# Kernel optimization log

Measured on AMD Instinct MI355X. Metric: run time of the kernel, lower is better.

Reference implementation:

```python
import jax, jax.numpy as jnp
import numpy as np
import math

BS, SEQ, HID = 1, 2048, 2048
NH, NKV, HD = 32, 8, 64
BASE = 10000.0


def rotate_half(x):
    x1, x2 = x[..., : x.shape[-1] // 2], x[..., x.shape[-1] // 2 :]
    return jnp.concatenate((-x2, x1), axis=-1)


def setup_inputs() -> dict:
    key = jax.random.key(0)
    ks = jax.random.split(key, 6)
    s = 0.02
    return {
        "x": jax.random.normal(ks[0], (BS, SEQ, HID), dtype=jnp.float32),
        "attention_mask": jnp.zeros((BS, SEQ), dtype=jnp.float32),
        "position_ids": jnp.broadcast_to(jnp.arange(SEQ, dtype=jnp.int64 if jax.config.jax_enable_x64 else jnp.int32), (BS, SEQ)),
        "wq": jax.random.normal(ks[1], (HID, NH * HD), dtype=jnp.float32) * s,
        "wk": jax.random.normal(ks[2], (HID, NKV * HD), dtype=jnp.float32) * s,
        "wv": jax.random.normal(ks[3], (HID, NKV * HD), dtype=jnp.float32) * s,
        "wo": jax.random.normal(ks[4], (NH * HD, HID), dtype=jnp.float32) * s,
    }


def reference(x, attention_mask, position_ids, wq, wk, wv, wo):
    bs, seq, _ = x.shape
    groups = NH // NKV

    q = (x @ wq).reshape(bs, seq, NH, HD).transpose(0, 2, 1, 3)   # [b,H,S,D]
    k = (x @ wk).reshape(bs, seq, NKV, HD).transpose(0, 2, 1, 3)  # [b,Hkv,S,D]
    v = (x @ wv).reshape(bs, seq, NKV, HD).transpose(0, 2, 1, 3)

    # rotary embedding
    inv_freq = 1.0 / (BASE ** (jnp.arange(0, HD, 2, dtype=jnp.float32) / HD))  # [D/2]
    freqs = position_ids.astype(jnp.float32)[:, :, None] * inv_freq[None, None, :]  # [b,S,D/2]
    emb = jnp.concatenate((freqs, freqs), axis=-1)               # [b,S,D]
    cos = jnp.cos(emb)[:, None, :, :].astype(x.dtype)            # [b,1,S,D]
    sin = jnp.sin(emb)[:, None, :, :].astype(x.dtype)
    q = q * cos + rotate_half(q) * sin
    k = k * cos + rotate_half(k) * sin

    # repeat_kv (GQA expand)
    k = jnp.repeat(k, groups, axis=1)  # [b,H,S,D]
    v = jnp.repeat(v, groups, axis=1)

    scores = jnp.einsum("bhqd,bhkd->bhqk", q, k) / math.sqrt(HD)
    scores = scores + attention_mask[:, None, None, :]
    attn = jax.nn.softmax(scores.astype(jnp.float32), axis=-1).astype(q.dtype)
    out = jnp.einsum("bhqk,bhkd->bhqd", attn, v)                 # [b,H,S,D]
    out = out.transpose(0, 2, 1, 3).reshape(bs, seq, NH * HD)
    return out @ wo
```

## Files before the change

kernel.cpp:

```cpp
#include <hip/hip_runtime.h>

#define SEQ 2048
#define HID 2048
#define NH  32
#define NKV 8
#define HD  64

typedef _Float16 f16;
typedef __attribute__((ext_vector_type(4))) _Float16 f16x4;
typedef __attribute__((ext_vector_type(8))) _Float16 f16x8;
typedef __attribute__((ext_vector_type(2))) __fp16   h16x2;
typedef __attribute__((ext_vector_type(4))) float    f32x4;

__device__ __forceinline__ f32x4 mfma_16x16x32(f16x8 a, f16x8 b, f32x4 c) {
    return __builtin_amdgcn_mfma_f32_16x16x32_f16(a, b, c, 0, 0, 0);
}

__device__ __forceinline__ void async16(const void* g, void* l) {
    __builtin_amdgcn_global_load_lds(
        (const __attribute__((address_space(1))) void*)g,
        (__attribute__((address_space(3))) void*)l,
        16, 0, 0);
}

__global__ void prep_all(const float* __restrict__ x,
                         const float* __restrict__ wq, const float* __restrict__ wk,
                         const float* __restrict__ wv, const float* __restrict__ wo,
                         f16* __restrict__ xb,
                         f16* __restrict__ Wcat, f16* __restrict__ woT) {
    __shared__ float tile[32][33];
    int z = blockIdx.z;
    int tx = threadIdx.x, ty = threadIdx.y;
    if (z == 4) {
        int idx = (blockIdx.y * 64 + blockIdx.x) * 256 + ty * 32 + tx;
        int i = idx * 4;
        float4 v = *(const float4*)(x + i);
        f16x4 o = { (f16)v.x, (f16)v.y, (f16)v.z, (f16)v.w };
        *(f16x4*)(xb + i) = o;
        return;
    }
    const float* src; f16* dst; int C;
    if      (z == 0) { src = wq; dst = Wcat;                         C = 2048; }
    else if (z == 1) { src = wk; dst = Wcat + (size_t)2048 * 2048;   C = 512;  }
    else if (z == 2) { src = wv; dst = Wcat + (size_t)2560 * 2048;   C = 512;  }
    else             { src = wo; dst = woT;                          C = 2048; }
    int c0 = blockIdx.x * 32, r0 = blockIdx.y * 32;
    if (c0 >= C) return;
#pragma unroll
    for (int i = 0; i < 32; i += 8)
        tile[ty + i][tx] = src[(size_t)(r0 + ty + i) * C + c0 + tx];
    __syncthreads();
#pragma unroll
    for (int i = 0; i < 32; i += 8)
        dst[(size_t)(c0 + ty + i) * 2048 + r0 + tx] = (f16)tile[tx][ty + i];
}

template <int MODE>
__global__ __launch_bounds__(256)
void gemm_bt(const f16* __restrict__ A, const f16* __restrict__ BT,
             float* __restrict__ Cf, f16* __restrict__ Q, f16* __restrict__ Kk,
             f16* __restrict__ VT, const int* __restrict__ pos,
             const float* __restrict__ mask, int N, int K) {
    __shared__ f16 As[2][64 * 64];
    __shared__ f16 Bs[2][128 * 64];
    int t = threadIdx.x;
    int w = t >> 6, lane = t & 63, quad = lane >> 4, l15 = lane & 15;
    int wm = w >> 1, wn = w & 1;
    int m0 = blockIdx.y * 64, n0 = blockIdx.x * 128;
    int sw = l15 & 7;

    int r8 = lane >> 3;
    int cc = (lane & 7) ^ r8;
    const f16* Ag0 = A  + (size_t)(m0 + w * 16 + r8) * K + cc * 8;
    const f16* Ag1 = Ag0 + (size_t)8 * K;
    const f16* Bg  = BT + (size_t)(n0 + w * 32 + r8) * K + cc * 8;

    f32x4 acc[2][4] = {};

    async16(Ag0, &As[0][w * 1024]);
    async16(Ag1, &As[0][w * 1024 + 512]);
#pragma unroll
    for (int g = 0; g < 4; g++)
        async16(Bg + (size_t)(8 * g) * K, &Bs[0][w * 2048 + g * 512]);
    __syncthreads();

    int b = 0;
    for (int kt = 64; kt <= K; kt += 64) {
        if (kt < K) {
            async16(Ag0 + kt, &As[b ^ 1][w * 1024]);
            async16(Ag1 + kt, &As[b ^ 1][w * 1024 + 512]);
#pragma unroll
            for (int g = 0; g < 4; g++)
                async16(Bg + (size_t)(8 * g) * K + kt, &Bs[b ^ 1][w * 2048 + g * 512]);
        }
        f16x8 af[2][2], bf[4][2];
#pragma unroll
        for (int mi = 0; mi < 2; mi++) {
            int row = wm * 32 + mi * 16 + l15;
#pragma unroll
            for (int kh = 0; kh < 2; kh++)
                af[mi][kh] = *(const f16x8*)(&As[b][row * 64 + ((kh * 4 + quad) ^ sw) * 8]);
        }
#pragma unroll
        for (int ni = 0; ni < 4; ni++) {
            int row = wn * 64 + ni * 16 + l15;
#pragma unroll
            for (int kh = 0; kh < 2; kh++)
                bf[ni][kh] = *(const f16x8*)(&Bs[b][row * 64 + ((kh * 4 + quad) ^ sw) * 8]);
        }
#pragma unroll
        for (int mi = 0; mi < 2; mi++)
#pragma unroll
            for (int ni = 0; ni < 4; ni++) {
                acc[mi][ni] = mfma_16x16x32(af[mi][0], bf[ni][0], acc[mi][ni]);
                acc[mi][ni] = mfma_16x16x32(af[mi][1], bf[ni][1], acc[mi][ni]);
            }
        __syncthreads();
        b ^= 1;
    }

    int rb  = m0 + wm * 32 + quad * 4;
    int cbh = n0 + wn * 64;
    if (MODE == 0) {
        if (cbh < (NH + NKV) * HD) {
            bool isQ = cbh < NH * HD;
            f16* dst = isQ ? (Q  + (size_t)(cbh >> 6) * SEQ * HD)
                           : (Kk + (size_t)((cbh - NH * HD) >> 6) * SEQ * HD);
            float scale = isQ ? 0.18033688011112042f : 1.0f;
            float fr[2];
#pragma unroll
            for (int ni = 0; ni < 2; ni++)
                fr[ni] = __builtin_amdgcn_exp2f(
                    (float)(ni * 16 + l15) * -0.41524101186092029f);
#pragma unroll
            for (int mi = 0; mi < 2; mi++)
#pragma unroll
                for (int r = 0; r < 4; r++) {
                    int row = rb + mi * 16 + r;
                    float pv = (float)pos[row];
#pragma unroll
                    for (int ni = 0; ni < 2; ni++) {
                        float sn, cs;
                        __sincosf(pv * fr[ni], &sn, &cs);
                        float x1 = acc[mi][ni][r], x2 = acc[mi][ni + 2][r];
                        int d = ni * 16 + l15;
                        dst[(size_t)row * HD + d]      = (f16)(scale * (x1 * cs - x2 * sn));
                        dst[(size_t)row * HD + d + 32] = (f16)(scale * (x2 * cs + x1 * sn));
                    }
                }
        } else {
            const float LOG2E = 1.4426950408889634f;
#pragma unroll
            for (int mi = 0; mi < 2; mi++) {
                float4 mv = *(const float4*)(mask + rb + mi * 16);
                float em[4];
#pragma unroll
                for (int r = 0; r < 4; r++)
                    em[r] = __builtin_amdgcn_exp2f((&mv.x)[r] * LOG2E);
#pragma unroll
                for (int ni = 0; ni < 4; ni++) {
                    int c2 = cbh - (NH + NKV) * HD + ni * 16 + l15;
                    f16x4 v4;
                    ((h16x2*)&v4)[0] = __builtin_amdgcn_cvt_pkrtz(
                        acc[mi][ni][0] * em[0], acc[mi][ni][1] * em[1]);
                    ((h16x2*)&v4)[1] = __builtin_amdgcn_cvt_pkrtz(
                        acc[mi][ni][2] * em[2], acc[mi][ni][3] * em[3]);
                    *(f16x4*)(VT + (size_t)c2 * SEQ + rb + mi * 16) = v4;
                }
            }
        }
    } else {
#pragma unroll
        for (int mi = 0; mi < 2; mi++)
#pragma unroll
            for (int ni = 0; ni < 4; ni++)
#pragma unroll
                for (int r = 0; r < 4; r++)
                    Cf[(size_t)(rb + mi * 16 + r) * N + cbh + ni * 16 + l15] =
                        acc[mi][ni][r];
    }
}

__global__ __launch_bounds__(256)
void attn_fused(const f16* __restrict__ Qb, const f16* __restrict__ Kb,
                const f16* __restrict__ VTb, const float* __restrict__ mask,
                f16* __restrict__ ctx) {
    __shared__ f16 Ks[2][64 * 64];
    __shared__ f16 Vs[2][64 * 64];
    __shared__ f16 Em[SEQ];

    int t = threadIdx.x, w = t >> 6, lane = t & 63, quad = lane >> 4, l15 = lane & 15;
    int h = blockIdx.y, kvh = h >> 2;
    int qbase = blockIdx.x * 128 + w * 32;
    const f16* Qh = Qb  + (size_t)h   * SEQ * HD;
    const f16* Kh = Kb  + (size_t)kvh * SEQ * HD;
    const f16* Vh = VTb + (size_t)kvh * HD * SEQ;
    int sw = l15 & 7;
    const float LOG2E = 1.4426950408889634f;

    {
        int idx = t * 8;
        float4 ma = *(const float4*)(mask + idx);
        float4 mb = *(const float4*)(mask + idx + 4);
        f16x8 e;
        ((h16x2*)&e)[0] = __builtin_amdgcn_cvt_pkrtz(
            __builtin_amdgcn_exp2f(ma.x * LOG2E), __builtin_amdgcn_exp2f(ma.y * LOG2E));
        ((h16x2*)&e)[1] = __builtin_amdgcn_cvt_pkrtz(
            __builtin_amdgcn_exp2f(ma.z * LOG2E), __builtin_amdgcn_exp2f(ma.w * LOG2E));
        ((h16x2*)&e)[2] = __builtin_amdgcn_cvt_pkrtz(
            __builtin_amdgcn_exp2f(mb.x * LOG2E), __builtin_amdgcn_exp2f(mb.y * LOG2E));
        ((h16x2*)&e)[3] = __builtin_amdgcn_cvt_pkrtz(
            __builtin_amdgcn_exp2f(mb.z * LOG2E), __builtin_amdgcn_exp2f(mb.w * LOG2E));
        *(f16x8*)(&Em[idx]) = e;
    }

    int r8 = lane >> 3;
    int cc = (lane & 7) ^ r8;
    int gk = 32 * (w >> 1) + 4 * (w & 1) + 8 * (r8 >> 2) + (r8 & 3);
    const f16* kg0 = Kh + (size_t)gk * HD + cc * 8;
    const f16* kg1 = kg0 + (size_t)16 * HD;
    const f16* vg0 = Vh + (size_t)(w * 16 + r8) * SEQ + cc * 8;
    const f16* vg1 = vg0 + 8 * SEQ;
    int lr0 = (w * 16) * 64, lr1 = (w * 16 + 8) * 64;

    async16(kg0, &Ks[0][lr0]);
    async16(kg1, &Ks[0][lr1]);
    async16(vg0, &Vs[0][lr0]);
    async16(vg1, &Vs[0][lr1]);

    f16x8 bq[2][2];
#pragma unroll
    for (int qg = 0; qg < 2; qg++)
#pragma unroll
        for (int ks = 0; ks < 2; ks++)
            bq[qg][ks] = *(const f16x8*)(Qh + (size_t)(qbase + qg * 16 + l15) * HD
                                            + ks * 32 + quad * 8);

    f32x4 o[4][2] = {};
    f32x4 ol[2]   = {};

    int c0 = (quad ^ sw) * 8, c1 = ((4 | quad) ^ sw) * 8;

    __syncthreads();
    int b = 0;

    for (int ktl = 0; ktl < SEQ / 64; ktl++) {
        if (ktl + 1 < SEQ / 64) {
            kg0 += 64 * HD; kg1 += 64 * HD; vg0 += 64; vg1 += 64;
            async16(kg0, &Ks[b ^ 1][lr0]);
            async16(kg1, &Ks[b ^ 1][lr1]);
            async16(vg0, &Vs[b ^ 1][lr0]);
            async16(vg1, &Vs[b ^ 1][lr1]);
        }
        const f16* Kb_ = &Ks[b][0];
        const f16* Vb_ = &Vs[b][0];

        f32x4 st[4][2] = {};
#pragma unroll
        for (int ni = 0; ni < 4; ni++) {
            const f16* kr = Kb_ + (ni * 16 + l15) * 64;
            f16x8 ak0 = *(const f16x8*)(kr + c0);
            f16x8 ak1 = *(const f16x8*)(kr + c1);
#pragma unroll
            for (int qg = 0; qg < 2; qg++) {
                st[ni][qg] = mfma_16x16x32(ak0, bq[qg][0], st[ni][qg]);
                st[ni][qg] = mfma_16x16x32(ak1, bq[qg][1], st[ni][qg]);
            }
        }
        f16x8 pb[2][2];
#pragma unroll
        for (int ni = 0; ni < 4; ni++)
#pragma unroll
            for (int qg = 0; qg < 2; qg++) {
                h16x2 lo = __builtin_amdgcn_cvt_pkrtz(
                    __builtin_amdgcn_exp2f(st[ni][qg][0]),
                    __builtin_amdgcn_exp2f(st[ni][qg][1]));
                h16x2 hi = __builtin_amdgcn_cvt_pkrtz(
                    __builtin_amdgcn_exp2f(st[ni][qg][2]),
                    __builtin_amdgcn_exp2f(st[ni][qg][3]));
                ((h16x2*)&pb[qg][ni >> 1])[(ni & 1) * 2]     = lo;
                ((h16x2*)&pb[qg][ni >> 1])[(ni & 1) * 2 + 1] = hi;
            }
        f16x8 em0 = *(const f16x8*)(&Em[ktl * 64 + quad * 8]);
        f16x8 em1 = *(const f16x8*)(&Em[ktl * 64 + 32 + quad * 8]);
#pragma unroll
        for (int qg = 0; qg < 2; qg++) {
            ol[qg] = mfma_16x16x32(em0, pb[qg][0], ol[qg]);
            ol[qg] = mfma_16x16x32(em1, pb[qg][1], ol[qg]);
        }
#pragma unroll
        for (int dt = 0; dt < 4; dt++) {
            const f16* vr = Vb_ + (dt * 16 + l15) * 64;
            f16x8 av0 = *(const f16x8*)(vr + c0);
            f16x8 av1 = *(const f16x8*)(vr + c1);
#pragma unroll
            for (int qg = 0; qg < 2; qg++) {
                o[dt][qg] = mfma_16x16x32(av0, pb[qg][0], o[dt][qg]);
                o[dt][qg] = mfma_16x16x32(av1, pb[qg][1], o[dt][qg]);
            }
        }
        __syncthreads();
        b ^= 1;
    }

    float linv[2] = { 1.0f / ol[0][0], 1.0f / ol[1][0] };

#pragma unroll
    for (int dt = 0; dt < 4; dt++)
#pragma unroll
        for (int qg = 0; qg < 2; qg++) {
            f16x4 v4;
            ((h16x2*)&v4)[0] = __builtin_amdgcn_cvt_pkrtz(
                o[dt][qg][0] * linv[qg], o[dt][qg][1] * linv[qg]);
            ((h16x2*)&v4)[1] = __builtin_amdgcn_cvt_pkrtz(
                o[dt][qg][2] * linv[qg], o[dt][qg][3] * linv[qg]);
            *(f16x4*)(ctx + (size_t)(qbase + qg * 16 + l15) * (NH * HD)
                          + h * 64 + dt * 16 + quad * 4) = v4;
        }
}

extern "C" void kernel_launch(void* const* d_in, const int* in_sizes, int n_in,
                              void* d_out, int out_size, void* d_ws, size_t ws_size,
                              hipStream_t stream) {
    const float* x    = (const float*)d_in[0];
    const float* mask = (const float*)d_in[1];
    const int*   pos  = (const int*)  d_in[2];
    const float* wq   = (const float*)d_in[3];
    const float* wk   = (const float*)d_in[4];
    const float* wv   = (const float*)d_in[5];
    const float* wo   = (const float*)d_in[6];
    float* out = (float*)d_out;

    char* ws = (char*)d_ws;
    f16* xb   = (f16*)(ws);
    f16* ctx  = (f16*)(ws);
    f16* Wcat = (f16*)(ws + ((size_t)8  << 20));
    f16* woT  = (f16*)(ws + ((size_t)20 << 20));
    f16* Qb   = (f16*)(ws + ((size_t)28 << 20));
    f16* Kb   = (f16*)(ws + ((size_t)36 << 20));
    f16* VTb  = (f16*)(ws + ((size_t)38 << 20));

    prep_all<<<dim3(64, 64, 5), dim3(32, 8), 0, stream>>>(
        x, wq, wk, wv, wo, xb, Wcat, woT);

    gemm_bt<0><<<dim3(3072 / 128, 2048 / 64), 256, 0, stream>>>(
        xb, Wcat, nullptr, Qb, Kb, VTb, pos, mask, 3072, 2048);

    attn_fused<<<dim3(SEQ / 128, NH), 256, 0, stream>>>(
        Qb, Kb, VTb, mask, ctx);

    gemm_bt<1><<<dim3(2048 / 128, 2048 / 64), 256, 0, stream>>>(
        ctx, woT, out, nullptr, nullptr, nullptr, nullptr, nullptr, 2048, 2048);
}
```

Before: 220.4 us.

## Split attention keys in two with 512-thread blocks and add combine kernel

The attention kernel now splits the key sequence into two halves along a new grid dimension. Each block handles 256 queries with 8 waves, and K and V tile loading is divided between wave groups. Each split writes unnormalized fp16 partial outputs and fp32 row sums. A new combine kernel adds the partials and normalizes them into the context buffer. The goal is to double the number of resident waves and share each K/V tile across more queries. The cost is an extra kernel launch and a round trip of the partial buffers through memory.

```diff
diff --git a/kernel.cpp b/kernel.cpp
--- a/kernel.cpp
+++ b/kernel.cpp
@@ -181,27 +181,28 @@
     }
 }
 
-__global__ __launch_bounds__(256)
+__global__ __launch_bounds__(512)
 void attn_fused(const f16* __restrict__ Qb, const f16* __restrict__ Kb,
                 const f16* __restrict__ VTb, const float* __restrict__ mask,
-                f16* __restrict__ ctx) {
+                f16* __restrict__ Opart, float* __restrict__ Lpart) {
     __shared__ f16 Ks[2][64 * 64];
     __shared__ f16 Vs[2][64 * 64];
-    __shared__ f16 Em[SEQ];
+    __shared__ f16 Em[SEQ / 2];
 
     int t = threadIdx.x, w = t >> 6, lane = t & 63, quad = lane >> 4, l15 = lane & 15;
-    int h = blockIdx.y, kvh = h >> 2;
-    int qbase = blockIdx.x * 128 + w * 32;
+    int h = blockIdx.y, kvh = h >> 2, split = blockIdx.z;
+    int qbase = blockIdx.x * 256 + w * 32;
+    int key0  = split * (SEQ / 2);
     const f16* Qh = Qb  + (size_t)h   * SEQ * HD;
     const f16* Kh = Kb  + (size_t)kvh * SEQ * HD;
     const f16* Vh = VTb + (size_t)kvh * HD * SEQ;
     int sw = l15 & 7;
     const float LOG2E = 1.4426950408889634f;
 
-    {
+    if (t < 128) {
         int idx = t * 8;
-        float4 ma = *(const float4*)(mask + idx);
-        float4 mb = *(const float4*)(mask + idx + 4);
+        float4 ma = *(const float4*)(mask + key0 + idx);
+        float4 mb = *(const float4*)(mask + key0 + idx + 4);
         f16x8 e;
         ((h16x2*)&e)[0] = __builtin_amdgcn_cvt_pkrtz(
             __builtin_amdgcn_exp2f(ma.x * LOG2E), __builtin_amdgcn_exp2f(ma.y * LOG2E));
@@ -216,17 +217,27 @@
 
     int r8 = lane >> 3;
     int cc = (lane & 7) ^ r8;
-    int gk = 32 * (w >> 1) + 4 * (w & 1) + 8 * (r8 >> 2) + (r8 & 3);
-    const f16* kg0 = Kh + (size_t)gk * HD + cc * 8;
-    const f16* kg1 = kg0 + (size_t)16 * HD;
-    const f16* vg0 = Vh + (size_t)(w * 16 + r8) * SEQ + cc * 8;
-    const f16* vg1 = vg0 + 8 * SEQ;
-    int lr0 = (w * 16) * 64, lr1 = (w * 16 + 8) * 64;
-
-    async16(kg0, &Ks[0][lr0]);
-    async16(kg1, &Ks[0][lr1]);
-    async16(vg0, &Vs[0][lr0]);
-    async16(vg1, &Vs[0][lr1]);
+    bool isK = w < 4;
+    int ws = isK ? w : (w - 4);
+    const f16* g0;
+    long gstep;
+    if (isK) {
+        int gk = 32 * (ws >> 1) + 4 * (ws & 1) + 8 * (r8 >> 2) + (r8 & 3);
+        g0 = Kh + (size_t)(key0 + gk) * HD + cc * 8;
+        gstep = (long)16 * HD;
+    } else {
+        g0 = Vh + (size_t)(ws * 16 + r8) * SEQ + key0 + cc * 8;
+        gstep = (long)8 * SEQ;
+    }
+    const f16* g1 = g0 + gstep;
+    long adv = isK ? (long)64 * HD : 64;
+    int lr0 = ws * 16 * 64, lr1 = lr0 + 8 * 64;
+
+    {
+        f16* dst = isK ? &Ks[0][0] : &Vs[0][0];
+        async16(g0, dst + lr0);
+        async16(g1, dst + lr1);
+    }
 
     f16x8 bq[2][2];
 #pragma unroll
@@ -244,13 +255,12 @@
     __syncthreads();
     int b = 0;
 
-    for (int ktl = 0; ktl < SEQ / 64; ktl++) {
-        if (ktl + 1 < SEQ / 64) {
-            kg0 += 64 * HD; kg1 += 64 * HD; vg0 += 64; vg1 += 64;
-            async16(kg0, &Ks[b ^ 1][lr0]);
-            async16(kg1, &Ks[b ^ 1][lr1]);
-            async16(vg0, &Vs[b ^ 1][lr0]);
-            async16(vg1, &Vs[b ^ 1][lr1]);
+    for (int ktl = 0; ktl < SEQ / 128; ktl++) {
+        if (ktl + 1 < SEQ / 128) {
+            g0 += adv; g1 += adv;
+            f16* dst = isK ? &Ks[b ^ 1][0] : &Vs[b ^ 1][0];
+            async16(g0, dst + lr0);
+            async16(g1, dst + lr1);
         }
         const f16* Kb_ = &Ks[b][0];
         const f16* Vb_ = &Vs[b][0];
@@ -303,20 +313,42 @@
         b ^= 1;
     }
 
-    float linv[2] = { 1.0f / ol[0][0], 1.0f / ol[1][0] };
-
+    if (quad == 0) {
+#pragma unroll
+        for (int qg = 0; qg < 2; qg++)
+            Lpart[((size_t)split * NH + h) * SEQ + qbase + qg * 16 + l15] =
+                ol[qg][0];
+    }
+    f16* Op = Opart + ((size_t)split * NH + h) * SEQ * HD;
 #pragma unroll
     for (int dt = 0; dt < 4; dt++)
 #pragma unroll
         for (int qg = 0; qg < 2; qg++) {
             f16x4 v4;
-            ((h16x2*)&v4)[0] = __builtin_amdgcn_cvt_pkrtz(
-                o[dt][qg][0] * linv[qg], o[dt][qg][1] * linv[qg]);
-            ((h16x2*)&v4)[1] = __builtin_amdgcn_cvt_pkrtz(
-                o[dt][qg][2] * linv[qg], o[dt][qg][3] * linv[qg]);
-            *(f16x4*)(ctx + (size_t)(qbase + qg * 16 + l15) * (NH * HD)
-                          + h * 64 + dt * 16 + quad * 4) = v4;
-        }
+            ((h16x2*)&v4)[0] = __builtin_amdgcn_cvt_pkrtz(o[dt][qg][0], o[dt][qg][1]);
+            ((h16x2*)&v4)[1] = __builtin_amdgcn_cvt_pkrtz(o[dt][qg][2], o[dt][qg][3]);
+            *(f16x4*)(Op + (size_t)(qbase + qg * 16 + l15) * HD
+                         + dt * 16 + quad * 4) = v4;
+        }
+}
+
+__global__ void attn_combine(const f16* __restrict__ O, const float* __restrict__ L,
+                             f16* __restrict__ ctx) {
+    int idx = blockIdx.x * 256 + threadIdx.x;
+    int c4  = idx & 511;
+    int row = idx >> 9;
+    int col = c4 * 4;
+    int h   = col >> 6;
+    float l = L[(size_t)h * SEQ + row] + L[(size_t)(NH + h) * SEQ + row];
+    const f16* o0 = O + ((size_t)h * SEQ + row) * HD + (col & 63);
+    const f16* o1 = o0 + (size_t)NH * SEQ * HD;
+    f16x4 a = *(const f16x4*)o0, b = *(const f16x4*)o1;
+    float inv = 1.0f / l;
+    f16x4 r;
+#pragma unroll
+    for (int j = 0; j < 4; j++)
+        r[j] = (f16)(((float)a[j] + (float)b[j]) * inv);
+    *(f16x4*)(ctx + (size_t)row * (NH * HD) + col) = r;
 }
 
 extern "C" void kernel_launch(void* const* d_in, const int* in_sizes, int n_in,
@@ -332,13 +364,15 @@
     float* out = (float*)d_out;
 
     char* ws = (char*)d_ws;
-    f16* xb   = (f16*)(ws);
-    f16* ctx  = (f16*)(ws);
-    f16* Wcat = (f16*)(ws + ((size_t)8  << 20));
-    f16* woT  = (f16*)(ws + ((size_t)20 << 20));
-    f16* Qb   = (f16*)(ws + ((size_t)28 << 20));
-    f16* Kb   = (f16*)(ws + ((size_t)36 << 20));
-    f16* VTb  = (f16*)(ws + ((size_t)38 << 20));
+    f16*   xb    = (f16*)(ws);
+    f16*   Wcat  = (f16*)(ws + ((size_t)8  << 20));
+    f16*   woT   = (f16*)(ws + ((size_t)20 << 20));
+    f16*   Qb    = (f16*)(ws + ((size_t)28 << 20));
+    f16*   Kb    = (f16*)(ws + ((size_t)36 << 20));
+    f16*   VTb   = (f16*)(ws + ((size_t)38 << 20));
+    f16*   Opart = (f16*)(ws);
+    float* Lpart = (float*)(ws + ((size_t)16 << 20));
+    f16*   ctx   = (f16*)(ws + ((size_t)28 << 20));
 
     prep_all<<<dim3(64, 64, 5), dim3(32, 8), 0, stream>>>(
         x, wq, wk, wv, wo, xb, Wcat, woT);
@@ -346,8 +380,9 @@
     gemm_bt<0><<<dim3(3072 / 128, 2048 / 64), 256, 0, stream>>>(
         xb, Wcat, nullptr, Qb, Kb, VTb, pos, mask, 3072, 2048);
 
-    attn_fused<<<dim3(SEQ / 128, NH), 256, 0, stream>>>(
-        Qb, Kb, VTb, mask, ctx);
+    attn_fused<<<dim3(SEQ / 256, NH, 2), 512, 0, stream>>>(
+        Qb, Kb, VTb, mask, Opart, Lpart);
+    attn_combine<<<SEQ * NH * HD / 4 / 256, 256, 0, stream>>>(Opart, Lpart, ctx);
 
     gemm_bt<1><<<dim3(2048 / 128, 2048 / 64), 256, 0, stream>>>(
         ctx, woT, out, nullptr, nullptr, nullptr, nullptr, nullptr, 2048, 2048);
```

Measured after the change: 206.5 us. 6.3% less time.
